# Optimization experiments

Measured on AMD Instinct MI355X. Metric: run time of the kernel, lower is better.

The kernel has to match this reference:

```python
import jax, jax.numpy as jnp
import numpy as np

D_MODEL = 1024
NHEAD = 8
HEAD_DIM = D_MODEL // NHEAD
D_FF = 4096
EPS_ATTN = 1e-6
EPS_LN = 1e-5


def _layernorm(x, g, b):
    mu = jnp.mean(x, axis=-1, keepdims=True)
    var = jnp.var(x, axis=-1, keepdims=True)
    return (x - mu) * jax.lax.rsqrt(var + EPS_LN) * g + b


def _linear_attention(q, k, v):
    # q,k,v: [N, L, H, D]
    Q = jax.nn.elu(q) + 1.0
    K = jax.nn.elu(k) + 1.0
    v_length = v.shape[1]
    v = v / v_length
    KV = jnp.einsum('nshd,nshv->nhdv', K, v)           # [N,H,D,D]
    Z = 1.0 / (jnp.einsum('nlhd,nhd->nlh', Q, K.sum(axis=1)) + EPS_ATTN)
    out = jnp.einsum('nlhd,nhdv,nlh->nlhv', Q, KV, Z) * v_length
    return out


def setup_inputs() -> dict:
    key = jax.random.key(0)
    ks = jax.random.split(key, 12)
    s = 1.0 / np.sqrt(D_MODEL)
    sf = 1.0 / np.sqrt(D_FF)
    return {
        'x': jax.random.normal(ks[0], (2, 4096, D_MODEL), jnp.float32),
        'wq': jax.random.normal(ks[1], (D_MODEL, D_MODEL), jnp.float32) * s,
        'wk': jax.random.normal(ks[2], (D_MODEL, D_MODEL), jnp.float32) * s,
        'wv': jax.random.normal(ks[3], (D_MODEL, D_MODEL), jnp.float32) * s,
        'w1': jax.random.normal(ks[4], (D_FF, D_MODEL), jnp.float32) * s,
        'b1': jnp.zeros((D_FF,), jnp.float32),
        'w2': jax.random.normal(ks[5], (D_MODEL, D_FF), jnp.float32) * sf,
        'b2': jnp.zeros((D_MODEL,), jnp.float32),
        'g1': jnp.ones((D_MODEL,), jnp.float32),
        'be1': jnp.zeros((D_MODEL,), jnp.float32),
        'g2': jnp.ones((D_MODEL,), jnp.float32),
        'be2': jnp.zeros((D_MODEL,), jnp.float32),
    }


def reference(x, wq, wk, wv, w1, b1, w2, b2, g1, be1, g2, be2):
    N, L, C = x.shape
    # pre-norm self attention
    x2 = _layernorm(x, g1, be1)
    q = (x2 @ wq.T).reshape(N, L, NHEAD, HEAD_DIM)
    k = (x2 @ wk.T).reshape(N, L, NHEAD, HEAD_DIM)
    v = (x2 @ wv.T).reshape(N, L, NHEAD, HEAD_DIM)
    msg = _linear_attention(q, k, v).reshape(N, L, C)
    x = x + msg
    # MLP block
    x2 = _layernorm(x, g2, be2)
    h = jax.nn.gelu(x2 @ w1.T + b1, approximate=False)
    x = x + (h @ w2.T + b2)
    return x
```

## Files before the change

### kernel.cpp

```cpp
#include <hip/hip_runtime.h>
#include <hip/hip_bf16.h>
#include <math.h>

typedef __bf16 bf16x8 __attribute__((ext_vector_type(8)));
typedef float f32x4 __attribute__((ext_vector_type(4)));

#define DEVI __device__ __forceinline__

DEVI void gload_lds16(const __bf16* g, __bf16* l) {
    __builtin_amdgcn_global_load_lds(
        (const __attribute__((address_space(1))) void*)g,
        (__attribute__((address_space(3))) void*)l, 16, 0, 0);
}

DEVI float erf_fast(float y) {
    const float ay = fabsf(y);
    const float t = __builtin_amdgcn_rcpf(fmaf(0.3275911f, ay, 1.0f));
    float p = 1.061405429f;
    p = fmaf(p, t, -1.453152027f);
    p = fmaf(p, t, 1.421413741f);
    p = fmaf(p, t, -0.284496736f);
    p = fmaf(p, t, 0.254829592f);
    p = p * t;
    const float e = exp2f(-y * y * 1.4426950408889634f);
    return copysignf(1.0f - p * e, y);
}

__global__ void sniff_kernel(const unsigned short* __restrict__ x, int* flags) {
    const int tid = threadIdx.x;
    const unsigned short u = x[tid * 2];
    const int e = (u >> 7) & 0xFF;
    const int zero = (u == 0) ? 1 : 0;
    const int sane = ((e >= 0x71 && e <= 0x8E) || ((u & 0x7FFF) == 0)) ? 1 : 0;
    const unsigned long long mz = __ballot(zero != 0);
    const unsigned long long ms = __ballot(sane != 0);
    __shared__ int wz[4], wsn[4];
    if ((tid & 63) == 0) { wz[tid >> 6] = __popcll(mz); wsn[tid >> 6] = __popcll(ms); }
    __syncthreads();
    if (tid == 0) {
        const int nz = wz[0] + wz[1] + wz[2] + wz[3];
        const int ns = wsn[0] + wsn[1] + wsn[2] + wsn[3];
        flags[0] = (nz >= 192 || ns < 128) ? 1 : 0;
    }
}

__global__ __launch_bounds__(256) void convert_kernel(const void* __restrict__ src,
                                                      __bf16* __restrict__ dst, int n,
                                                      const int* __restrict__ flags) {
    const int i = (blockIdx.x * 256 + threadIdx.x) * 8;
    if (i >= n) return;
    if (flags[0]) {
        const float* s = (const float*)src;
        bf16x8 o;
#pragma unroll
        for (int j = 0; j < 8; j++) o[j] = (__bf16)s[i + j];
        *(bf16x8*)(dst + i) = o;
    } else {
        *(uint4*)(dst + i) = *(const uint4*)((const __bf16*)src + i);
    }
}

struct CvtJobs {
    const float* s[11];
    __bf16* d[11];
    int n[11];
    int b0[11];
};
struct CvtLn1 {
    CvtJobs J;
    const float* x;
    const float* g;
    const float* b;
    __bf16* out;
    int bcvt;
};
__global__ __launch_bounds__(256) void cvt_ln1_kernel(CvtLn1 P) {
    const int bid = blockIdx.x;
    const int tid = threadIdx.x;
    if (bid < P.bcvt) {
        int j = 0;
#pragma unroll
        for (int k = 1; k < 11; k++)
            if (bid >= P.J.b0[k]) j = k;
        const int i = (bid - P.J.b0[j]) * 2048 + tid * 8;
        if (i >= P.J.n[j]) return;
        const float* s = P.J.s[j] + i;
        bf16x8 o;
#pragma unroll
        for (int t = 0; t < 8; t++) o[t] = (__bf16)s[t];
        *(bf16x8*)(P.J.d[j] + i) = o;
        return;
    }
    const size_t row = (size_t)(bid - P.bcvt);
    const float* xr = P.x + row * 1024;
    float v[4];
#pragma unroll
    for (int i = 0; i < 4; i++) v[i] = xr[tid * 4 + i];
    float s = v[0] + v[1] + v[2] + v[3];
    float s2 = v[0] * v[0] + v[1] * v[1] + v[2] * v[2] + v[3] * v[3];
#pragma unroll
    for (int m = 32; m >= 1; m >>= 1) {
        s += __shfl_xor(s, m, 64);
        s2 += __shfl_xor(s2, m, 64);
    }
    __shared__ float rs[4], rs2[4];
    const int wave = tid >> 6, lane = tid & 63;
    if (lane == 0) { rs[wave] = s; rs2[wave] = s2; }
    __syncthreads();
    s = rs[0] + rs[1] + rs[2] + rs[3];
    s2 = rs2[0] + rs2[1] + rs2[2] + rs2[3];
    const float mu = s * (1.0f / 1024.0f);
    const float var = s2 * (1.0f / 1024.0f) - mu * mu;
    const float inv = rsqrtf(var + 1e-5f);
#pragma unroll
    for (int i = 0; i < 4; i++) {
        const int c = tid * 4 + i;
        P.out[row * 1024 + c] = (__bf16)((v[i] - mu) * inv * P.g[c] + P.b[c]);
    }
}

template <typename T>
__global__ __launch_bounds__(256) void ln_kernel(const T* __restrict__ x,
                                                 const __bf16* __restrict__ g,
                                                 const __bf16* __restrict__ b,
                                                 __bf16* __restrict__ out) {
    const size_t row = blockIdx.x;
    const T* xr = x + row * 1024;
    const int tid = threadIdx.x;
    float v[4];
#pragma unroll
    for (int i = 0; i < 4; i++) v[i] = (float)xr[tid * 4 + i];
    float s = v[0] + v[1] + v[2] + v[3];
    float s2 = v[0] * v[0] + v[1] * v[1] + v[2] * v[2] + v[3] * v[3];
#pragma unroll
    for (int m = 32; m >= 1; m >>= 1) {
        s += __shfl_xor(s, m, 64);
        s2 += __shfl_xor(s2, m, 64);
    }
    __shared__ float rs[4], rs2[4];
    const int wave = tid >> 6, lane = tid & 63;
    if (lane == 0) { rs[wave] = s; rs2[wave] = s2; }
    __syncthreads();
    s = rs[0] + rs[1] + rs[2] + rs[3];
    s2 = rs2[0] + rs2[1] + rs2[2] + rs2[3];
    const float mu = s * (1.0f / 1024.0f);
    const float var = s2 * (1.0f / 1024.0f) - mu * mu;
    const float inv = rsqrtf(var + 1e-5f);
#pragma unroll
    for (int i = 0; i < 4; i++) {
        const int c = tid * 4 + i;
        out[row * 1024 + c] = (__bf16)((v[i] - mu) * inv * (float)g[c] + (float)b[c]);
    }
}

enum { EP_NONE = 0, EP_ELU1 = 1, EP_BIAS_GELU = 2, EP_BIAS_RES = 3, EP_QKV = 4 };

#define READMM(RA, RB)                                                            \
    do {                                                                          \
        bf16x8 af_[BM / 32], bfv_[4];                                             \
        _Pragma("unroll") for (int i_ = 0; i_ < BM / 32; i_++)                    \
            af_[i_] = *(const bf16x8*)&RA[(wm * (BM / 2) + i_ * 16 + lm) * 32 + swz]; \
        _Pragma("unroll") for (int j_ = 0; j_ < 4; j_++)                          \
            bfv_[j_] = *(const bf16x8*)&RB[(wn * 64 + j_ * 16 + lm) * 32 + swz];  \
        _Pragma("unroll") for (int i_ = 0; i_ < BM / 32; i_++)                    \
            _Pragma("unroll") for (int j_ = 0; j_ < 4; j_++)                      \
                acc[i_][j_] = __builtin_amdgcn_mfma_f32_16x16x32_bf16(            \
                    af_[i_], bfv_[j_], acc[i_][j_], 0, 0, 0);                     \
    } while (0)

#define KBODY(RA, RB, SA, SB, TS)                                  \
    do {                                                           \
        if constexpr (BM == 128)                                   \
            asm volatile("s_waitcnt vmcnt(4)" ::: "memory");       \
        else                                                       \
            asm volatile("s_waitcnt vmcnt(3)" ::: "memory");       \
        __builtin_amdgcn_s_barrier();                              \
        __builtin_amdgcn_sched_barrier(0);                         \
        if ((TS) < nt) {                                           \
            const int k0_ = (TS) << 5;                             \
            gload_lds16(pa0 + k0_, &SA[tid * 8]);                  \
            if constexpr (BM == 128)                               \
                gload_lds16(pa1 + k0_, &SA[2048 + tid * 8]);       \
            gload_lds16(pb0 + k0_, &SB[tid * 8]);                  \
            gload_lds16(pb1 + k0_, &SB[2048 + tid * 8]);           \
        }                                                          \
        __builtin_amdgcn_s_setprio(1);                             \
        READMM(RA, RB);                                            \
        __builtin_amdgcn_s_setprio(0);                             \
    } while (0)

template <int EP, int BM, typename OutT>
__global__ __launch_bounds__(256, 3) void gemm_bt(
    const __bf16* __restrict__ A, const __bf16* __restrict__ B,
    const __bf16* __restrict__ bias, const float* __restrict__ resid,
    OutT* __restrict__ C, int M, int N, int K) {
    const int gx = gridDim.x, gy = gridDim.y;
    int bm = blockIdx.y, bn = blockIdx.x;
    {
        const int nwg = gx * gy;
        if ((gx & 7) == 0 && (nwg & 63) == 0) {
            const int bid = bm * gx + bn;
            const int perx = nwg >> 3;
            const int gid = (bid & 7) * perx + (bid >> 3);
            const int stg = gid >> 6, pos = gid & 63;
            const int stw = gx >> 3;
            bm = (stg / stw) * 8 + (pos >> 3);
            bn = (stg % stw) * 8 + (pos & 7);
        }
    }
    const int tid = threadIdx.x;
    const int wave = tid >> 6, lane = tid & 63;
    const int wm = wave & 1, wn = wave >> 1;
    const int lm = lane & 15, lq = lane >> 4;
    const int swz = (lq ^ ((lm >> 1) & 3)) * 8;

    __shared__ __align__(16) __bf16 As0[BM * 32];
    __shared__ __align__(16) __bf16 As1[BM * 32];
    __shared__ __align__(16) __bf16 As2[BM * 32];
    __shared__ __align__(16) __bf16 Bs0[128 * 32];
    __shared__ __align__(16) __bf16 Bs1[128 * 32];
    __shared__ __align__(16) __bf16 Bs2[128 * 32];

    f32x4 acc[BM / 32][4] = {};

    const int sr = tid >> 2;
    const int sc = (((tid & 3) ^ ((tid >> 3) & 3)) << 3);

    const __bf16* pa0 = A + (size_t)(bm * BM + sr) * K + sc;
    const __bf16* pa1 = pa0 + (size_t)(BM == 128 ? 64 : 0) * K;
    const __bf16* pb0 = B + (size_t)(bn * 128 + sr) * K + sc;
    const __bf16* pb1 = pb0 + (size_t)64 * K;

    const int nt = K >> 5;

    gload_lds16(pa0, &As0[tid * 8]);
    if constexpr (BM == 128) gload_lds16(pa1, &As0[2048 + tid * 8]);
    gload_lds16(pb0, &Bs0[tid * 8]);
    gload_lds16(pb1, &Bs0[2048 + tid * 8]);
    if (nt > 1) {
        gload_lds16(pa0 + 32, &As1[tid * 8]);
        if constexpr (BM == 128) gload_lds16(pa1 + 32, &As1[2048 + tid * 8]);
        gload_lds16(pb0 + 32, &Bs1[tid * 8]);
        gload_lds16(pb1 + 32, &Bs1[2048 + tid * 8]);
    }

    int t = 0;
    for (; t + 2 < nt; t += 3) {
        KBODY(As0, Bs0, As2, Bs2, t + 2);
        KBODY(As1, Bs1, As0, Bs0, t + 3);
        KBODY(As2, Bs2, As1, Bs1, t + 4);
    }
    if (t < nt) {
        asm volatile("s_waitcnt vmcnt(0)" ::: "memory");
        __builtin_amdgcn_s_barrier();
        __builtin_amdgcn_sched_barrier(0);
        READMM(As0, Bs0);
        t++;
        if (t < nt) { READMM(As1, Bs1); }
    }

    const int row0 = bm * BM + wm * (BM / 2);
    const int col0 = bn * 128 + wn * 64;
#pragma unroll
    for (int i = 0; i < BM / 32; i++) {
#pragma unroll
        for (int j = 0; j < 4; j++) {
            const int col = col0 + j * 16 + lm;
#pragma unroll
            for (int r = 0; r < 4; r++) {
                const int row = row0 + i * 16 + lq * 4 + r;
                float v = acc[i][j][r];
                if (EP == EP_QKV) {
                    float vv = (col < 2048) ? ((v > 0.0f) ? (v + 1.0f) : expf(v)) : v;
                    __bf16* dst = (col < 1024) ? (__bf16*)C
                                : (col < 2048) ? (__bf16*)const_cast<__bf16*>(bias)
                                               : (__bf16*)const_cast<float*>(resid);
                    dst[(size_t)row * 1024 + (col & 1023)] = (__bf16)vv;
                } else {
                    if (EP == EP_ELU1) {
                        v = (v > 0.0f) ? (v + 1.0f) : expf(v);
                    } else if (EP == EP_BIAS_GELU) {
                        v += (float)bias[col];
                        v = 0.5f * v * (1.0f + erf_fast(v * 0.70710678118654752f));
                    } else if (EP == EP_BIAS_RES) {
                        v += (float)bias[col];
                        v += resid[(size_t)row * N + col];
                    }
                    C[(size_t)row * N + col] = (OutT)v;
                }
            }
        }
    }
}

__global__ __launch_bounds__(256) void kv_kernel(const __bf16* __restrict__ Kf,
                                                 const __bf16* __restrict__ Vf,
                                                 float* __restrict__ pkv,
                                                 float* __restrict__ pks) {
    const int nh = blockIdx.x, sc = blockIdx.y;
    const int n = nh >> 3, h = nh & 7;
    const int tid = threadIdx.x;
    const int tv = tid & 15, td = tid >> 4;
    __shared__ __align__(16) __bf16 Kt[32 * 128];
    __shared__ __align__(16) __bf16 Vt[32 * 128];
    float acc[8][8] = {};
    float ks[8] = {};
    const size_t rowbase = (size_t)n * 4096 + (size_t)sc * 256;
    for (int s0 = 0; s0 < 256; s0 += 32) {
#pragma unroll
        for (int rep = 0; rep < 2; rep++) {
            const int s = tid + rep * 256;
            const int r = s >> 4, cs = (s & 15) * 8;
            const size_t gidx = (rowbase + s0 + r) * 1024 + h * 128 + cs;
            *(bf16x8*)&Kt[r * 128 + cs] = *(const bf16x8*)&Kf[gidx];
            *(bf16x8*)&Vt[r * 128 + cs] = *(const bf16x8*)&Vf[gidx];
        }
        __syncthreads();
#pragma unroll 4
        for (int s = 0; s < 32; s++) {
            const bf16x8 k8 = *(const bf16x8*)&Kt[s * 128 + td * 8];
            const bf16x8 v8 = *(const bf16x8*)&Vt[s * 128 + tv * 8];
            float kk[8], vv[8];
#pragma unroll
            for (int i = 0; i < 8; i++) { kk[i] = (float)k8[i]; vv[i] = (float)v8[i]; }
#pragma unroll
            for (int i = 0; i < 8; i++) {
                ks[i] += kk[i];
#pragma unroll
                for (int j = 0; j < 8; j++) acc[i][j] += kk[i] * vv[j];
            }
        }
        __syncthreads();
    }
    float* dst = pkv + ((size_t)sc * 16 + nh) * 16384;
#pragma unroll
    for (int i = 0; i < 8; i++)
#pragma unroll
        for (int j = 0; j < 8; j++)
            dst[(td * 8 + i) * 128 + tv * 8 + j] = acc[i][j];
    if (tv == 0) {
        float* ds2 = pks + ((size_t)sc * 16 + nh) * 128;
#pragma unroll
        for (int i = 0; i < 8; i++) ds2[td * 8 + i] = ks[i];
    }
}

__global__ __launch_bounds__(256) void kv_reduce(const float* __restrict__ pkv,
                                                 const float* __restrict__ pks,
                                                 __bf16* __restrict__ kvb,
                                                 float* __restrict__ ksf) {
    const int idx = blockIdx.x * 256 + threadIdx.x;
    float s = 0.0f;
#pragma unroll
    for (int c = 0; c < 16; c++) s += pkv[(size_t)c * 262144 + idx];
    kvb[idx] = (__bf16)s;
    if (idx < 2048) {
        float t = 0.0f;
#pragma unroll
        for (int c = 0; c < 16; c++) t += pks[c * 2048 + idx];
        ksf[idx] = t;
    }
}

template <typename XT>
__global__ __launch_bounds__(256, 2) void attn_out_kernel(
    const XT* __restrict__ x, const __bf16* __restrict__ Qf,
    const __bf16* __restrict__ kvb, const float* __restrict__ ksf,
    float* __restrict__ xmid) {
    const int nh = blockIdx.x, lc = blockIdx.y;
    const int n = nh >> 3, h = nh & 7;
    const int tid = threadIdx.x;
    __shared__ __align__(16) __bf16 KVs[128 * 128];
    __shared__ __align__(16) __bf16 Qs[64 * 128];
    __shared__ float Ks[128];
    const __bf16* kv = kvb + (size_t)nh * 16384;
    for (int i = tid * 8; i < 16384; i += 2048)
        *(bf16x8*)&KVs[i] = *(const bf16x8*)&kv[i];
    const size_t gr0 = (size_t)n * 4096 + (size_t)lc * 64;
#pragma unroll
    for (int rep = 0; rep < 4; rep++) {
        const int s = tid + rep * 256;
        const int r = s >> 4, cs = (s & 15) * 8;
        *(bf16x8*)&Qs[r * 128 + cs] = *(const bf16x8*)&Qf[(gr0 + r) * 1024 + h * 128 + cs];
    }
    if (tid < 128) Ks[tid] = ksf[(size_t)nh * 128 + tid];
    __syncthreads();
    const int tv = (tid & 15) * 8;
    const int tr0 = (tid >> 4) * 4;
    float acc[4][8] = {};
    float zs[4] = {};
    for (int d = 0; d < 128; d++) {
        const bf16x8 kv8 = *(const bf16x8*)&KVs[d * 128 + tv];
        const float ksd = Ks[d];
        float kf[8];
#pragma unroll
        for (int j = 0; j < 8; j++) kf[j] = (float)kv8[j];
#pragma unroll
        for (int rr = 0; rr < 4; rr++) {
            const float q = (float)Qs[(tr0 + rr) * 128 + d];
            zs[rr] += q * ksd;
#pragma unroll
            for (int j = 0; j < 8; j++) acc[rr][j] += q * kf[j];
        }
    }
#pragma unroll
    for (int rr = 0; rr < 4; rr++) {
        const size_t gi = (gr0 + tr0 + rr) * 1024 + h * 128 + tv;
        const float z = 1.0f / (zs[rr] + 1e-6f);
        const XT* xr = x + gi;
#pragma unroll
        for (int j = 0; j < 8; j++) xmid[gi + j] = (float)xr[j] + acc[rr][j] * z;
    }
}

extern "C" void kernel_launch(void* const* d_in, const int* in_sizes, int n_in,
                              void* d_out, int out_size, void* d_ws, size_t ws_size,
                              hipStream_t stream) {
    float* out = (float*)d_out;
    char* ws = (char*)d_ws;

    const int nx = 8388608, nw = 1048576, nw1 = 4194304, nb1 = 4096, ng = 1024;
    size_t off = 0;
    __bf16* cx   = (__bf16*)(ws + off); off += (size_t)nx * 2;
    __bf16* cwq  = (__bf16*)(ws + off); off += (size_t)nw * 2;
    __bf16* cwk  = (__bf16*)(ws + off); off += (size_t)nw * 2;
    __bf16* cwv  = (__bf16*)(ws + off); off += (size_t)nw * 2;
    __bf16* cw1  = (__bf16*)(ws + off); off += (size_t)nw1 * 2;
    __bf16* cb1  = (__bf16*)(ws + off); off += (size_t)nb1 * 2;
    __bf16* cw2  = (__bf16*)(ws + off); off += (size_t)nw1 * 2;
    __bf16* cb2  = (__bf16*)(ws + off); off += (size_t)ng * 2;
    __bf16* cg1  = (__bf16*)(ws + off); off += (size_t)ng * 2;
    __bf16* cbe1 = (__bf16*)(ws + off); off += (size_t)ng * 2;
    __bf16* cg2  = (__bf16*)(ws + off); off += (size_t)ng * 2;
    __bf16* cbe2 = (__bf16*)(ws + off); off += (size_t)ng * 2;
    int* flags = (int*)(ws + off); off += 64;

    char* PB = ws + off;
    __bf16* x2   = (__bf16*)(PB);
    float*  pkv  = (float*)(PB + 33554432);
    __bf16* Qf   = (__bf16*)(PB + 16777216);
    __bf16* hbuf = (__bf16*)(PB + 16777216);
    __bf16* Kf   = (__bf16*)(PB + 50331648);
    __bf16* Vf   = (__bf16*)(PB + 67108864);
    float*  xmid = (float*)(PB + 50331648);
    float*  pks  = (float*)(PB + 83886080);
    float*  ksf  = (float*)(PB + 84017152);
    __bf16* kvb  = (__bf16*)(PB + 84287488);
    __bf16* hbig = (__bf16*)(PB + 84811776);
    const size_t need_single = (size_t)(PB - ws) + 84811776 + (size_t)8192 * 4096 * 2;
    const bool single_mlp = ws_size >= need_single;

    const bool is_f32 = (in_sizes[0] == nx * 4);
    if (is_f32) {
        CvtLn1 P;
        const float* srcs[11] = {(const float*)d_in[1], (const float*)d_in[2],
                                 (const float*)d_in[3], (const float*)d_in[4],
                                 (const float*)d_in[5], (const float*)d_in[6],
                                 (const float*)d_in[7], (const float*)d_in[8],
                                 (const float*)d_in[9], (const float*)d_in[10],
                                 (const float*)d_in[11]};
        __bf16* dsts[11] = {cwq, cwk, cwv, cw1, cb1, cw2, cb2, cg1, cbe1, cg2, cbe2};
        int ns[11] = {nw, nw, nw, nw1, nb1, nw1, ng, ng, ng, ng, ng};
        int b = 0;
        for (int k = 0; k < 11; k++) {
            P.J.s[k] = srcs[k]; P.J.d[k] = dsts[k]; P.J.n[k] = ns[k]; P.J.b0[k] = b;
            b += (ns[k] + 2047) / 2048;
        }
        P.x = (const float*)d_in[0];
        P.g = (const float*)d_in[8];
        P.b = (const float*)d_in[9];
        P.out = x2;
        P.bcvt = b;
        cvt_ln1_kernel<<<b + 8192, 256, 0, stream>>>(P);
    } else {
        sniff_kernel<<<1, 256, 0, stream>>>((const unsigned short*)d_in[0], flags);
        convert_kernel<<<nx / 2048, 256, 0, stream>>>(d_in[0], cx, nx, flags);
        convert_kernel<<<nw / 2048, 256, 0, stream>>>(d_in[1], cwq, nw, flags);
        convert_kernel<<<nw / 2048, 256, 0, stream>>>(d_in[2], cwk, nw, flags);
        convert_kernel<<<nw / 2048, 256, 0, stream>>>(d_in[3], cwv, nw, flags);
        convert_kernel<<<nw1 / 2048, 256, 0, stream>>>(d_in[4], cw1, nw1, flags);
        convert_kernel<<<2, 256, 0, stream>>>(d_in[5], cb1, nb1, flags);
        convert_kernel<<<nw1 / 2048, 256, 0, stream>>>(d_in[6], cw2, nw1, flags);
        convert_kernel<<<1, 256, 0, stream>>>(d_in[7], cb2, ng, flags);
        convert_kernel<<<1, 256, 0, stream>>>(d_in[8], cg1, ng, flags);
        convert_kernel<<<1, 256, 0, stream>>>(d_in[9], cbe1, ng, flags);
        convert_kernel<<<1, 256, 0, stream>>>(d_in[10], cg2, ng, flags);
        convert_kernel<<<1, 256, 0, stream>>>(d_in[11], cbe2, ng, flags);
        ln_kernel<__bf16><<<8192, 256, 0, stream>>>(cx, cg1, cbe1, x2);
    }

    gemm_bt<EP_QKV, 128, __bf16><<<dim3(3072 / 128, 8192 / 128), 256, 0, stream>>>(
        x2, cwq, (const __bf16*)Kf, (const float*)Vf, Qf, 8192, 3072, 1024);

    kv_kernel<<<dim3(16, 16), 256, 0, stream>>>(Kf, Vf, pkv, pks);
    kv_reduce<<<1024, 256, 0, stream>>>(pkv, pks, kvb, ksf);

    if (is_f32)
        attn_out_kernel<float><<<dim3(16, 64), 256, 0, stream>>>(
            (const float*)d_in[0], Qf, kvb, ksf, xmid);
    else
        attn_out_kernel<__bf16><<<dim3(16, 64), 256, 0, stream>>>(
            cx, Qf, kvb, ksf, xmid);

    ln_kernel<float><<<8192, 256, 0, stream>>>(xmid, cg2, cbe2, x2);
    if (single_mlp) {
        gemm_bt<EP_BIAS_GELU, 128, __bf16><<<dim3(4096 / 128, 8192 / 128), 256, 0, stream>>>(
            x2, cw1, cb1, nullptr, hbig, 8192, 4096, 1024);
        gemm_bt<EP_BIAS_RES, 128, float><<<dim3(1024 / 128, 8192 / 128), 256, 0, stream>>>(
            hbig, cw2, cb2, xmid, out, 8192, 1024, 4096);
    } else {
        for (int c = 0; c < 2; c++) {
            const size_t ro = (size_t)c * 4096;
            gemm_bt<EP_BIAS_GELU, 128, __bf16><<<dim3(4096 / 128, 4096 / 128), 256, 0, stream>>>(
                x2 + ro * 1024, cw1, cb1, nullptr, hbuf, 4096, 4096, 1024);
            gemm_bt<EP_BIAS_RES, 64, float><<<dim3(1024 / 128, 4096 / 64), 256, 0, stream>>>(
                hbuf, cw2, cb2, xmid + ro * 1024, out + ro * 1024, 4096, 1024, 4096);
        }
    }
}
```

Before: 395.2 us.

## Add 256x256-tile 512-thread GEMM for QKV and FFN1 projections

Adds a new GEMM kernel with 256x256 output tiles, 8 waves, and double-buffered direct global-to-LDS loads. It uses a phased schedule with barriers, setprio around the MFMA blocks, and an XCD-aware block swizzle. The kernel replaces the 128-tile GEMM for the QKV projection and, on the single-MLP path, for the first FFN layer. The aim is more operand reuse per loaded byte and better L2 locality. In exchange it uses 128 KB of LDS and far more accumulator registers, which limits occupancy to one block per CU, and the grids shrink (384 and 512 blocks).

```diff
diff --git a/kernel.cpp b/kernel.cpp
--- a/kernel.cpp
+++ b/kernel.cpp
@@ -154,6 +154,136 @@
 }
 
 enum { EP_NONE = 0, EP_ELU1 = 1, EP_BIAS_GELU = 2, EP_BIAS_RES = 3, EP_QKV = 4 };
+
+#define STG4(DA, DB, KOFF)                                  \
+    do {                                                    \
+        gload_lds16(sA0 + (KOFF), &DA[tid * 8]);            \
+        gload_lds16(sA1 + (KOFF), &DA[4096 + tid * 8]);     \
+        gload_lds16(sB0 + (KOFF), &DB[tid * 8]);            \
+        gload_lds16(sB1 + (KOFF), &DB[4096 + tid * 8]);     \
+    } while (0)
+
+#define PH256(RA, RB, FRB, READB, BV, DO_STG, SDA, SDB, KOFF, VMN)             \
+    do {                                                                       \
+        if ((VMN) == 4) asm volatile("s_waitcnt vmcnt(4)" ::: "memory");       \
+        else if ((VMN) == 0) asm volatile("s_waitcnt vmcnt(0)" ::: "memory");  \
+        __builtin_amdgcn_s_barrier();                                          \
+        __builtin_amdgcn_sched_barrier(0);                                     \
+        if (DO_STG) STG4(SDA, SDB, KOFF);                                      \
+        bf16x8 a_[4];                                                          \
+        if (READB)                                                             \
+            _Pragma("unroll") for (int f_ = 0; f_ < 4; f_++)                   \
+                BV[f_] = *(const bf16x8*)&RB[boff[f_]];                        \
+        _Pragma("unroll") for (int f_ = 0; f_ < 4; f_++)                       \
+            a_[f_] = *(const bf16x8*)&RA[aoff[(FRB) + f_]];                    \
+        __builtin_amdgcn_s_setprio(1);                                         \
+        _Pragma("unroll") for (int f_ = 0; f_ < 4; f_++)                       \
+            _Pragma("unroll") for (int c_ = 0; c_ < 4; c_++)                   \
+                acc[(FRB) + f_][c_] = __builtin_amdgcn_mfma_f32_16x16x32_bf16( \
+                    a_[f_], BV[c_], acc[(FRB) + f_][c_], 0, 0, 0);             \
+        __builtin_amdgcn_s_setprio(0);                                         \
+    } while (0)
+
+#define TILE256(AX0, AX1, BX0, BX1, AY0, AY1, BY0, BY1, KT, DO_STG, VM1)       \
+    do {                                                                       \
+        PH256(AX0, BX0, 0, 1, b0, DO_STG, AY0, BY0, (KT) * 64, 4);             \
+        PH256(AX1, BX1, 0, 1, b1, DO_STG, AY1, BY1, (KT) * 64 + 32, VM1);      \
+        PH256(AX0, BX0, 4, 0, b0, 0, AY0, BY0, 0, -1);                         \
+        PH256(AX1, BX1, 4, 0, b1, 0, AY1, BY1, 0, -1);                         \
+    } while (0)
+
+template <int EP>
+__global__ __launch_bounds__(512) void gemm256(
+    const __bf16* __restrict__ A, const __bf16* __restrict__ B,
+    const __bf16* __restrict__ bias, __bf16* __restrict__ out2,
+    __bf16* __restrict__ out3, __bf16* __restrict__ C, int M, int N, int K) {
+    const int gx = gridDim.x, gy = gridDim.y;
+    int bm = blockIdx.y, bn = blockIdx.x;
+    {
+        const int nwg = gx * gy;
+        const int bid = bm * gx + bn;
+        if ((gx & 7) == 0 && (nwg & 63) == 0) {
+            const int perx = nwg >> 3;
+            const int gid = (bid & 7) * perx + (bid >> 3);
+            const int stg = gid >> 6, pos = gid & 63;
+            const int stw = gx >> 3;
+            bm = (stg / stw) * 8 + (pos >> 3);
+            bn = (stg % stw) * 8 + (pos & 7);
+        } else if ((nwg & 7) == 0) {
+            const int perx = nwg >> 3;
+            const int gid = (bid & 7) * perx + (bid >> 3);
+            bm = gid / gx;
+            bn = gid % gx;
+        }
+    }
+    const int tid = threadIdx.x;
+    const int wave = tid >> 6, lane = tid & 63;
+    const int wr = wave >> 2, wc = wave & 3;
+    const int lm = lane & 15, lq = lane >> 4;
+
+    __shared__ __align__(16) __bf16 A0k0[8192];
+    __shared__ __align__(16) __bf16 A0k1[8192];
+    __shared__ __align__(16) __bf16 B0k0[8192];
+    __shared__ __align__(16) __bf16 B0k1[8192];
+    __shared__ __align__(16) __bf16 A1k0[8192];
+    __shared__ __align__(16) __bf16 A1k1[8192];
+    __shared__ __align__(16) __bf16 B1k0[8192];
+    __shared__ __align__(16) __bf16 B1k1[8192];
+
+    f32x4 acc[8][4] = {};
+    bf16x8 b0[4], b1[4];
+
+    const int swz = (lq ^ ((lm >> 1) & 3)) << 3;
+    int aoff[8], boff[4];
+#pragma unroll
+    for (int fr = 0; fr < 8; fr++) aoff[fr] = (wr * 128 + fr * 16 + lm) * 32 + swz;
+#pragma unroll
+    for (int fc = 0; fc < 4; fc++) boff[fc] = (wc * 64 + fc * 16 + lm) * 32 + swz;
+
+    const int srow = tid >> 2;
+    const int sg = (((tid & 3) ^ ((tid >> 3) & 3)) << 3);
+    const __bf16* sA0 = A + (size_t)(bm * 256 + srow) * K + sg;
+    const __bf16* sA1 = sA0 + (size_t)128 * K;
+    const __bf16* sB0 = B + (size_t)(bn * 256 + srow) * K + sg;
+    const __bf16* sB1 = sB0 + (size_t)128 * K;
+
+    const int nt = K >> 6;
+
+    STG4(A0k0, B0k0, 0);
+    STG4(A0k1, B0k1, 32);
+
+    int t = 0;
+    for (; t + 2 < nt; t += 2) {
+        TILE256(A0k0, A0k1, B0k0, B0k1, A1k0, A1k1, B1k0, B1k1, t + 1, 1, 4);
+        TILE256(A1k0, A1k1, B1k0, B1k1, A0k0, A0k1, B0k0, B0k1, t + 2, 1, 4);
+    }
+    TILE256(A0k0, A0k1, B0k0, B0k1, A1k0, A1k1, B1k0, B1k1, t + 1, 1, 4);
+    TILE256(A1k0, A1k1, B1k0, B1k1, A0k0, A0k1, B0k0, B0k1, 0, 0, 0);
+
+    const int rowb = bm * 256 + wr * 128 + lq * 4;
+    const int colb = bn * 256 + wc * 64 + lm;
+#pragma unroll
+    for (int fr = 0; fr < 8; fr++) {
+#pragma unroll
+        for (int fc = 0; fc < 4; fc++) {
+            const int col = colb + fc * 16;
+#pragma unroll
+            for (int r = 0; r < 4; r++) {
+                const int row = rowb + fr * 16 + r;
+                float v = acc[fr][fc][r];
+                if (EP == EP_QKV) {
+                    float vv = (col < 2048) ? ((v > 0.0f) ? (v + 1.0f) : expf(v)) : v;
+                    __bf16* dst = (col < 1024) ? C : (col < 2048) ? out2 : out3;
+                    dst[(size_t)row * 1024 + (col & 1023)] = (__bf16)vv;
+                } else {
+                    v += (float)bias[col];
+                    v = 0.5f * v * (1.0f + erf_fast(v * 0.70710678118654752f));
+                    C[(size_t)row * N + col] = (__bf16)v;
+                }
+            }
+        }
+    }
+}
 
 #define READMM(RA, RB)                                                            \
     do {                                                                          \
@@ -489,8 +619,8 @@
         ln_kernel<__bf16><<<8192, 256, 0, stream>>>(cx, cg1, cbe1, x2);
     }
 
-    gemm_bt<EP_QKV, 128, __bf16><<<dim3(3072 / 128, 8192 / 128), 256, 0, stream>>>(
-        x2, cwq, (const __bf16*)Kf, (const float*)Vf, Qf, 8192, 3072, 1024);
+    gemm256<EP_QKV><<<dim3(3072 / 256, 8192 / 256), 512, 0, stream>>>(
+        x2, cwq, nullptr, Kf, Vf, Qf, 8192, 3072, 1024);
 
     kv_kernel<<<dim3(16, 16), 256, 0, stream>>>(Kf, Vf, pkv, pks);
     kv_reduce<<<1024, 256, 0, stream>>>(pkv, pks, kvb, ksf);
@@ -504,8 +634,8 @@
 
     ln_kernel<float><<<8192, 256, 0, stream>>>(xmid, cg2, cbe2, x2);
     if (single_mlp) {
-        gemm_bt<EP_BIAS_GELU, 128, __bf16><<<dim3(4096 / 128, 8192 / 128), 256, 0, stream>>>(
-            x2, cw1, cb1, nullptr, hbig, 8192, 4096, 1024);
+        gemm256<EP_BIAS_GELU><<<dim3(4096 / 256, 8192 / 256), 512, 0, stream>>>(
+            x2, cw1, cb1, nullptr, nullptr, hbig, 8192, 4096, 1024);
         gemm_bt<EP_BIAS_RES, 128, float><<<dim3(1024 / 128, 8192 / 128), 256, 0, stream>>>(
             hbig, cw2, cb2, xmid, out, 8192, 1024, 4096);
     } else {
```

New measurement: 421.6 us. +6.7%, slower.
